# Kernel tuning notes

Hardware: AMD Instinct MI355X
Metric: run time of the kernel (lower is better)

## Reference

```python
import jax, jax.numpy as jnp
import numpy as np

H = 512          # hidden_size == input_size
K = 32768        # number of child cell inputs (lattice merge fan-in)


def setup_inputs() -> dict:
    key = jax.random.key(0)
    ks = jax.random.split(key, 8)
    s = 1.0 / np.sqrt(H)  # keep matmul outputs O(1)
    return {
        "input_": jax.random.normal(ks[0], (1, H), dtype=jnp.float32),
        "c_input": jax.random.normal(ks[1], (K, H), dtype=jnp.float32),
        "h_0": jax.random.normal(ks[2], (1, H), dtype=jnp.float32),
        "c_0": jax.random.normal(ks[3], (1, H), dtype=jnp.float32),
        "weight_ih": jax.random.normal(ks[4], (H, 3 * H), dtype=jnp.float32) * s,
        "weight_hh": jax.random.normal(ks[5], (H, 3 * H), dtype=jnp.float32) * s,
        "bias": jnp.zeros((3 * H,), dtype=jnp.float32),
        "alpha_weight_ih": jax.random.normal(ks[6], (H, H), dtype=jnp.float32) * s,
        "alpha_weight_hh": jax.random.normal(ks[7], (H, H), dtype=jnp.float32) * s,
    }


def reference(input_, c_input, h_0, c_0, weight_ih, weight_hh, bias,
              alpha_weight_ih, alpha_weight_hh):
    # Gate pre-activations: addmm(bias, h_0, W_hh) + input_ @ W_ih  -> [1, 3H]
    gates = h_0 @ weight_hh + bias + input_ @ weight_ih
    i, o, g = jnp.split(gates, 3, axis=1)        # each [1, H]
    i = jax.nn.sigmoid(i)
    o = jax.nn.sigmoid(o)
    g = jnp.tanh(g)

    # Variable-child softmax-weighted cell merge (non-empty c_input branch)
    alpha_wi = input_ @ alpha_weight_ih          # [1, H], broadcast over K
    alpha_wh = c_input @ alpha_weight_hh         # [K, H]
    alpha = jax.nn.sigmoid(alpha_wi + alpha_wh)  # [K, H]

    logits = jnp.concatenate([i, alpha], axis=0)  # [K+1, H]
    w = jnp.exp(logits)
    w = w / (w.sum(axis=0, keepdims=True) + 1e-12)

    merge = jnp.concatenate([g, c_input], axis=0)  # [K+1, H]
    c_1 = (merge * w).sum(axis=0, keepdims=True)   # [1, H]
    h_1 = o * jnp.tanh(c_1)                        # [1, H]
    return h_1, c_1
```

## Files before the change

### kernel.cpp

```cpp
#include <hip/hip_runtime.h>
#include <hip/hip_bf16.h>
#include <stdint.h>

#define Hdim 512
#define KC   32768

typedef __hip_bfloat16 bf16;
typedef __attribute__((ext_vector_type(8))) short short8;
typedef __attribute__((ext_vector_type(4))) float float4v;

__device__ __forceinline__ unsigned int pack_bf16_trunc(float e0, float e1) {
  union { float f; unsigned int u; } a, b;
  a.f = e0; b.f = e1;
  return __builtin_amdgcn_perm(b.u, a.u, 0x07060302u);
}

__global__ __launch_bounds__(256) void prep_wt_kernel(
    const float* __restrict__ input_, const float* __restrict__ h_0,
    const float* __restrict__ w_ih, const float* __restrict__ w_hh,
    const float* __restrict__ a_w_ih, const float* __restrict__ a_w_hh,
    float* __restrict__ gates, float* __restrict__ awi, bf16* __restrict__ wt) {
  __shared__ float sh[64 * 65];
  const int t = threadIdx.x;
  if (blockIdx.x < 128) {
    const int b  = blockIdx.x;
    const int jt = b & 31, dc = b >> 5;
    const int lane = t & 63, wv = t >> 6;
    float* h0s = sh;
    float* ins = sh + 128;
    float* red = sh + 256;
    if (t < 128) { h0s[t] = h_0[dc * 128 + t]; ins[t] = input_[dc * 128 + t]; }
    __syncthreads();
    float acc = 0.f;
    if (jt < 24) {
      const int j = jt * 64 + lane;
#pragma unroll 4
      for (int i = 0; i < 32; ++i) {
        const int dl = wv * 32 + i;
        const size_t d = dc * 128 + dl;
        acc += h0s[dl] * w_hh[d * 1536 + j] + ins[dl] * w_ih[d * 1536 + j];
      }
    } else {
      const int j = (jt - 24) * 64 + lane;
#pragma unroll 4
      for (int i = 0; i < 32; ++i) {
        const int dl = wv * 32 + i;
        const size_t d = dc * 128 + dl;
        acc += ins[dl] * a_w_ih[d * Hdim + j];
      }
    }
    red[wv * 64 + lane] = acc;
    __syncthreads();
    if (t < 64) {
      float s = red[t] + red[64 + t] + red[128 + t] + red[192 + t];
      if (jt < 24) atomicAdd(&gates[jt * 64 + t], s);
      else         atomicAdd(&awi[(jt - 24) * 64 + t], s);
    }
  } else {
    const int b = blockIdx.x - 128;
    const int d0 = (b & 7) * 64, h0 = (b >> 3) * 64;
    const int tx = t & 63, tw = t >> 6;
    float (*tile)[65] = (float (*)[65])sh;
#pragma unroll
    for (int r = 0; r < 16; ++r) {
      const int row = r * 4 + tw;
      tile[row][tx] = a_w_hh[(size_t)(d0 + row) * Hdim + h0 + tx];
    }
    __syncthreads();
#pragma unroll
    for (int r = 0; r < 16; ++r) {
      const int row = r * 4 + tw;
      wt[(size_t)(h0 + row) * Hdim + d0 + tx] = __float2bfloat16(tile[tx][row]);
    }
  }
}

__global__ __launch_bounds__(256) void gemm_reduce_kernel(
    const float* __restrict__ c_input, const bf16* __restrict__ WT,
    const float* __restrict__ awi,
    float* __restrict__ pw, float* __restrict__ pwc) {
  __shared__ __align__(16) bf16 As[128 * 64];
  __shared__ __align__(16) bf16 Bs[128 * 64];
  __shared__ float red_w[2][128];
  __shared__ float red_wc[2][128];

  const int tid  = threadIdx.x;
  const int lane = tid & 63;
  const int wave = tid >> 6;
  const int wm   = wave & 1;
  const int wn   = wave >> 1;
  const int lm   = lane & 15;
  const int lq   = lane >> 4;

  const int id     = blockIdx.x;
  const int kk_idx = ((id >> 5) << 3) | (id & 7);
  const int h_idx  = (id >> 3) & 3;
  const int kk0 = kk_idx * 128;
  const int h0  = h_idx * 128;

  float4v acc[4][4];
#pragma unroll
  for (int i = 0; i < 4; ++i)
#pragma unroll
    for (int j = 0; j < 4; ++j)
      acc[i][j] = (float4v){0.f, 0.f, 0.f, 0.f};

  char* AsB = (char*)As;
  char* BsB = (char*)Bs;

  for (int d0 = 0; d0 < Hdim; d0 += 64) {
#pragma unroll
    for (int j = 0; j < 8; ++j) {
      const int f = j * 256 + tid;
      const int row = f >> 4, sub = f & 15;
      float4v v = *(const float4v*)(c_input + (size_t)(kk0 + row) * Hdim + d0 + sub * 4);
      unsigned long long p = (unsigned long long)pack_bf16_trunc(v[0], v[1])
                           | ((unsigned long long)pack_bf16_trunc(v[2], v[3]) << 32);
      *(unsigned long long*)(AsB + row * 128 + (((sub >> 1) ^ (row & 7)) * 16) + (sub & 1) * 8) = p;
    }
#pragma unroll
    for (int r = 0; r < 4; ++r) {
      const int row = r * 32 + wave * 8 + (lane >> 3);
      const int g   = lane & 7;
      short8 wv8 = *(const short8*)(WT + (size_t)(h0 + row) * Hdim + d0 + g * 8);
      *(short8*)(BsB + row * 128 + ((g ^ (lane >> 3)) * 16)) = wv8;
    }
    __syncthreads();

#pragma unroll
    for (int ks = 0; ks < 2; ++ks) {
      short8 a[4], b[4];
#pragma unroll
      for (int mt = 0; mt < 4; ++mt) {
        const int row = wm * 64 + mt * 16 + lm;
        a[mt] = *(const short8*)(AsB + row * 128 + (((ks * 4 + lq) ^ (lm & 7)) * 16));
      }
#pragma unroll
      for (int nt = 0; nt < 4; ++nt) {
        const int row = wn * 64 + nt * 16 + lm;
        b[nt] = *(const short8*)(BsB + row * 128 + (((ks * 4 + lq) ^ (lm & 7)) * 16));
      }
#pragma unroll
      for (int mt = 0; mt < 4; ++mt)
#pragma unroll
        for (int nt = 0; nt < 4; ++nt)
          acc[mt][nt] = __builtin_amdgcn_mfma_f32_16x16x32_bf16(a[mt], b[nt], acc[mt][nt], 0, 0, 0);
    }
    __syncthreads();
  }

  float awi_l[4];
#pragma unroll
  for (int nt = 0; nt < 4; ++nt)
    awi_l[nt] = awi[h0 + wn * 64 + nt * 16 + lm];

  float sw[4] = {0.f, 0.f, 0.f, 0.f}, swc[4] = {0.f, 0.f, 0.f, 0.f};
#pragma unroll
  for (int nt = 0; nt < 4; ++nt) {
    const int h = h0 + wn * 64 + nt * 16 + lm;
#pragma unroll
    for (int mt = 0; mt < 4; ++mt) {
      const int kkb = kk0 + wm * 64 + mt * 16 + lq * 4;
#pragma unroll
      for (int r = 0; r < 4; ++r) {
        float v = acc[mt][nt][r] + awi_l[nt];
        float aval = 1.f / (1.f + __expf(-v));
        float e = __expf(aval);
        float c = c_input[(size_t)(kkb + r) * Hdim + h];
        sw[nt]  += e;
        swc[nt] += e * c;
      }
    }
  }
#pragma unroll
  for (int nt = 0; nt < 4; ++nt) {
    sw[nt]  += __shfl_xor(sw[nt], 16, 64);
    sw[nt]  += __shfl_xor(sw[nt], 32, 64);
    swc[nt] += __shfl_xor(swc[nt], 16, 64);
    swc[nt] += __shfl_xor(swc[nt], 32, 64);
  }
  if (lq == 0) {
#pragma unroll
    for (int nt = 0; nt < 4; ++nt) {
      red_w[wm][wn * 64 + nt * 16 + lm]  = sw[nt];
      red_wc[wm][wn * 64 + nt * 16 + lm] = swc[nt];
    }
  }
  __syncthreads();
  if (tid < 128) {
    pw[(size_t)kk_idx * Hdim + h0 + tid]  = red_w[0][tid] + red_w[1][tid];
    pwc[(size_t)kk_idx * Hdim + h0 + tid] = red_wc[0][tid] + red_wc[1][tid];
  }
}

__global__ __launch_bounds__(256) void finalize_kernel(
    const float* __restrict__ pw, const float* __restrict__ pwc,
    const float* __restrict__ gates, const float* __restrict__ bias,
    float* __restrict__ out) {
  __shared__ float rsw[4][64], rswc[4][64];
  const int t = threadIdx.x;
  const int hl = t & 63, q = t >> 6;
  const int hh = blockIdx.x * 64 + hl;
  float sw = 0.f, swc = 0.f;
#pragma unroll 4
  for (int kb = q * 64; kb < q * 64 + 64; ++kb) {
    sw  += pw[(size_t)kb * Hdim + hh];
    swc += pwc[(size_t)kb * Hdim + hh];
  }
  rsw[q][hl] = sw; rswc[q][hl] = swc;
  __syncthreads();
  if (t < 64) {
    const int h = blockIdx.x * 64 + t;
    sw  = rsw[0][t] + rsw[1][t] + rsw[2][t] + rsw[3][t];
    swc = rswc[0][t] + rswc[1][t] + rswc[2][t] + rswc[3][t];
    float ipre = gates[h] + bias[h];
    float opre = gates[Hdim + h] + bias[Hdim + h];
    float gpre = gates[2 * Hdim + h] + bias[2 * Hdim + h];
    float ei = expf(1.f / (1.f + expf(-ipre)));
    float g  = tanhf(gpre);
    float o  = 1.f / (1.f + expf(-opre));
    float denom = ei + sw + 1e-12f;
    float c1 = (ei * g + swc) / denom;
    float h1 = o * tanhf(c1);
    out[h]        = h1;
    out[Hdim + h] = c1;
  }
}

extern "C" void kernel_launch(void* const* d_in, const int* in_sizes, int n_in,
                              void* d_out, int out_size, void* d_ws, size_t ws_size,
                              hipStream_t stream) {
  const float* input_  = (const float*)d_in[0];
  const float* c_input = (const float*)d_in[1];
  const float* h_0     = (const float*)d_in[2];
  const float* w_ih    = (const float*)d_in[4];
  const float* w_hh    = (const float*)d_in[5];
  const float* bias    = (const float*)d_in[6];
  const float* a_w_ih  = (const float*)d_in[7];
  const float* a_w_hh  = (const float*)d_in[8];

  char* ws = (char*)d_ws;
  float* pw    = (float*)ws;
  float* pwc   = (float*)(ws + 512 * 1024);
  float* gates = (float*)(ws + 1024 * 1024);
  float* awi   = (float*)(ws + 1024 * 1024 + 6144);
  bf16*  WT    = (bf16*)(ws + 1024 * 1024 + 8192);

  hipMemsetAsync(ws + 1024 * 1024, 0, 8192, stream);
  hipLaunchKernelGGL(prep_wt_kernel, dim3(192), dim3(256), 0, stream,
                     input_, h_0, w_ih, w_hh, a_w_ih, a_w_hh, gates, awi, WT);
  hipLaunchKernelGGL(gemm_reduce_kernel, dim3(1024), dim3(256), 0, stream,
                     c_input, WT, awi, pw, pwc);
  hipLaunchKernelGGL(finalize_kernel, dim3(8), dim3(256), 0, stream,
                     pw, pwc, gates, bias, (float*)d_out);
}
```

Measured before the change: 152.6 us.

## Drop LDS staging in GEMM, load MFMA operands directly from global

The GEMM-reduce kernel drops its shared-memory tiling. Each wave now loads its 16-row A fragment straight from c_input, converts it to bf16, and reads B fragments for a 256-wide N slice directly from global memory. This removes the LDS round trips and the per-step barriers. In exchange, reuse of B across waves now relies on L1/L2 instead of LDS, and the number of partial-sum rows doubles. The prep kernel is also rewritten to compute the gate vectors with full 1024-thread blocks and no atomics, which removes the memset, and the finalize kernel reduces the partials with 16 waves.

```diff
diff --git a/kernel.cpp b/kernel.cpp
--- a/kernel.cpp
+++ b/kernel.cpp
@@ -15,61 +15,52 @@
   return __builtin_amdgcn_perm(b.u, a.u, 0x07060302u);
 }
 
-__global__ __launch_bounds__(256) void prep_wt_kernel(
+__global__ __launch_bounds__(1024) void prep_wt_kernel(
     const float* __restrict__ input_, const float* __restrict__ h_0,
     const float* __restrict__ w_ih, const float* __restrict__ w_hh,
     const float* __restrict__ a_w_ih, const float* __restrict__ a_w_hh,
     float* __restrict__ gates, float* __restrict__ awi, bf16* __restrict__ wt) {
-  __shared__ float sh[64 * 65];
   const int t = threadIdx.x;
-  if (blockIdx.x < 128) {
-    const int b  = blockIdx.x;
-    const int jt = b & 31, dc = b >> 5;
-    const int lane = t & 63, wv = t >> 6;
-    float* h0s = sh;
-    float* ins = sh + 128;
-    float* red = sh + 256;
-    if (t < 128) { h0s[t] = h_0[dc * 128 + t]; ins[t] = input_[dc * 128 + t]; }
+  if (blockIdx.x < 8) {
+    __shared__ float h0s[Hdim], ins[Hdim];
+    __shared__ float red[4][256];
+    const int js = t & 255, ds = t >> 8;
+    for (int i = t; i < Hdim; i += 1024) { h0s[i] = h_0[i]; ins[i] = input_[i]; }
     __syncthreads();
+    const int j = blockIdx.x * 256 + js;
     float acc = 0.f;
-    if (jt < 24) {
-      const int j = jt * 64 + lane;
-#pragma unroll 4
-      for (int i = 0; i < 32; ++i) {
-        const int dl = wv * 32 + i;
-        const size_t d = dc * 128 + dl;
-        acc += h0s[dl] * w_hh[d * 1536 + j] + ins[dl] * w_ih[d * 1536 + j];
-      }
+    if (j < 1536) {
+#pragma unroll 8
+      for (int d = ds * 128; d < ds * 128 + 128; ++d)
+        acc += h0s[d] * w_hh[(size_t)d * 1536 + j] + ins[d] * w_ih[(size_t)d * 1536 + j];
     } else {
-      const int j = (jt - 24) * 64 + lane;
-#pragma unroll 4
-      for (int i = 0; i < 32; ++i) {
-        const int dl = wv * 32 + i;
-        const size_t d = dc * 128 + dl;
-        acc += ins[dl] * a_w_ih[d * Hdim + j];
-      }
-    }
-    red[wv * 64 + lane] = acc;
+      const int jj = j - 1536;
+#pragma unroll 8
+      for (int d = ds * 128; d < ds * 128 + 128; ++d)
+        acc += ins[d] * a_w_ih[(size_t)d * Hdim + jj];
+    }
+    red[ds][js] = acc;
     __syncthreads();
-    if (t < 64) {
-      float s = red[t] + red[64 + t] + red[128 + t] + red[192 + t];
-      if (jt < 24) atomicAdd(&gates[jt * 64 + t], s);
-      else         atomicAdd(&awi[(jt - 24) * 64 + t], s);
+    if (t < 256) {
+      const int jo = blockIdx.x * 256 + t;
+      float s = red[0][t] + red[1][t] + red[2][t] + red[3][t];
+      if (jo < 1536) gates[jo] = s;
+      else           awi[jo - 1536] = s;
     }
   } else {
-    const int b = blockIdx.x - 128;
+    __shared__ float tile[64][65];
+    const int b = blockIdx.x - 8;
     const int d0 = (b & 7) * 64, h0 = (b >> 3) * 64;
     const int tx = t & 63, tw = t >> 6;
-    float (*tile)[65] = (float (*)[65])sh;
-#pragma unroll
-    for (int r = 0; r < 16; ++r) {
-      const int row = r * 4 + tw;
+#pragma unroll
+    for (int r = 0; r < 4; ++r) {
+      const int row = r * 16 + tw;
       tile[row][tx] = a_w_hh[(size_t)(d0 + row) * Hdim + h0 + tx];
     }
     __syncthreads();
 #pragma unroll
-    for (int r = 0; r < 16; ++r) {
-      const int row = r * 4 + tw;
+    for (int r = 0; r < 4; ++r) {
+      const int row = r * 16 + tw;
       wt[(size_t)(h0 + row) * Hdim + d0 + tx] = __float2bfloat16(tile[tx][row]);
     }
   }
@@ -79,131 +70,95 @@
     const float* __restrict__ c_input, const bf16* __restrict__ WT,
     const float* __restrict__ awi,
     float* __restrict__ pw, float* __restrict__ pwc) {
-  __shared__ __align__(16) bf16 As[128 * 64];
-  __shared__ __align__(16) bf16 Bs[128 * 64];
-  __shared__ float red_w[2][128];
-  __shared__ float red_wc[2][128];
+  __shared__ float red_w[4][256];
+  __shared__ float red_wc[4][256];
 
   const int tid  = threadIdx.x;
   const int lane = tid & 63;
-  const int wave = tid >> 6;
-  const int wm   = wave & 1;
-  const int wn   = wave >> 1;
+  const int wv   = tid >> 6;
   const int lm   = lane & 15;
   const int lq   = lane >> 4;
 
   const int id     = blockIdx.x;
-  const int kk_idx = ((id >> 5) << 3) | (id & 7);
-  const int h_idx  = (id >> 3) & 3;
-  const int kk0 = kk_idx * 128;
-  const int h0  = h_idx * 128;
-
-  float4v acc[4][4];
-#pragma unroll
-  for (int i = 0; i < 4; ++i)
-#pragma unroll
-    for (int j = 0; j < 4; ++j)
-      acc[i][j] = (float4v){0.f, 0.f, 0.f, 0.f};
-
-  char* AsB = (char*)As;
-  char* BsB = (char*)Bs;
-
-  for (int d0 = 0; d0 < Hdim; d0 += 64) {
-#pragma unroll
-    for (int j = 0; j < 8; ++j) {
-      const int f = j * 256 + tid;
-      const int row = f >> 4, sub = f & 15;
-      float4v v = *(const float4v*)(c_input + (size_t)(kk0 + row) * Hdim + d0 + sub * 4);
-      unsigned long long p = (unsigned long long)pack_bf16_trunc(v[0], v[1])
-                           | ((unsigned long long)pack_bf16_trunc(v[2], v[3]) << 32);
-      *(unsigned long long*)(AsB + row * 128 + (((sub >> 1) ^ (row & 7)) * 16) + (sub & 1) * 8) = p;
-    }
+  const int kk_idx = ((id >> 4) << 3) | (id & 7);
+  const int h_idx  = (id >> 3) & 1;
+  const int m0 = kk_idx * 64 + wv * 16;
+  const int n0 = h_idx * 256;
+
+  float4v acc[16];
+#pragma unroll
+  for (int i = 0; i < 16; ++i) acc[i] = (float4v){0.f, 0.f, 0.f, 0.f};
+
+  const float* arow = c_input + (size_t)(m0 + lm) * Hdim;
+
+#pragma unroll 2
+  for (int ks = 0; ks < 16; ++ks) {
+    const int kb = ks * 32 + lq * 8;
+    float4v a0 = *(const float4v*)(arow + kb);
+    float4v a1 = *(const float4v*)(arow + kb + 4);
+    union { unsigned int u[4]; short8 s; } af;
+    af.u[0] = pack_bf16_trunc(a0[0], a0[1]);
+    af.u[1] = pack_bf16_trunc(a0[2], a0[3]);
+    af.u[2] = pack_bf16_trunc(a1[0], a1[1]);
+    af.u[3] = pack_bf16_trunc(a1[2], a1[3]);
+    short8 bf0[8], bf1[8];
+#pragma unroll
+    for (int nt = 0; nt < 8; ++nt)
+      bf0[nt] = *(const short8*)(WT + (size_t)(n0 + nt * 16 + lm) * Hdim + kb);
+#pragma unroll
+    for (int nt = 0; nt < 8; ++nt)
+      acc[nt] = __builtin_amdgcn_mfma_f32_16x16x32_bf16(af.s, bf0[nt], acc[nt], 0, 0, 0);
+#pragma unroll
+    for (int nt = 0; nt < 8; ++nt)
+      bf1[nt] = *(const short8*)(WT + (size_t)(n0 + (nt + 8) * 16 + lm) * Hdim + kb);
+#pragma unroll
+    for (int nt = 0; nt < 8; ++nt)
+      acc[nt + 8] = __builtin_amdgcn_mfma_f32_16x16x32_bf16(af.s, bf1[nt], acc[nt + 8], 0, 0, 0);
+  }
+
+#pragma unroll
+  for (int nt = 0; nt < 16; ++nt) {
+    const int n = n0 + nt * 16 + lm;
+    const float aw = awi[n];
+    float sw = 0.f, swc = 0.f;
 #pragma unroll
     for (int r = 0; r < 4; ++r) {
-      const int row = r * 32 + wave * 8 + (lane >> 3);
-      const int g   = lane & 7;
-      short8 wv8 = *(const short8*)(WT + (size_t)(h0 + row) * Hdim + d0 + g * 8);
-      *(short8*)(BsB + row * 128 + ((g ^ (lane >> 3)) * 16)) = wv8;
-    }
-    __syncthreads();
-
-#pragma unroll
-    for (int ks = 0; ks < 2; ++ks) {
-      short8 a[4], b[4];
-#pragma unroll
-      for (int mt = 0; mt < 4; ++mt) {
-        const int row = wm * 64 + mt * 16 + lm;
-        a[mt] = *(const short8*)(AsB + row * 128 + (((ks * 4 + lq) ^ (lm & 7)) * 16));
-      }
-#pragma unroll
-      for (int nt = 0; nt < 4; ++nt) {
-        const int row = wn * 64 + nt * 16 + lm;
-        b[nt] = *(const short8*)(BsB + row * 128 + (((ks * 4 + lq) ^ (lm & 7)) * 16));
-      }
-#pragma unroll
-      for (int mt = 0; mt < 4; ++mt)
-#pragma unroll
-        for (int nt = 0; nt < 4; ++nt)
-          acc[mt][nt] = __builtin_amdgcn_mfma_f32_16x16x32_bf16(a[mt], b[nt], acc[mt][nt], 0, 0, 0);
-    }
-    __syncthreads();
-  }
-
-  float awi_l[4];
-#pragma unroll
-  for (int nt = 0; nt < 4; ++nt)
-    awi_l[nt] = awi[h0 + wn * 64 + nt * 16 + lm];
-
-  float sw[4] = {0.f, 0.f, 0.f, 0.f}, swc[4] = {0.f, 0.f, 0.f, 0.f};
-#pragma unroll
-  for (int nt = 0; nt < 4; ++nt) {
-    const int h = h0 + wn * 64 + nt * 16 + lm;
-#pragma unroll
-    for (int mt = 0; mt < 4; ++mt) {
-      const int kkb = kk0 + wm * 64 + mt * 16 + lq * 4;
-#pragma unroll
-      for (int r = 0; r < 4; ++r) {
-        float v = acc[mt][nt][r] + awi_l[nt];
-        float aval = 1.f / (1.f + __expf(-v));
-        float e = __expf(aval);
-        float c = c_input[(size_t)(kkb + r) * Hdim + h];
-        sw[nt]  += e;
-        swc[nt] += e * c;
-      }
-    }
-  }
-#pragma unroll
-  for (int nt = 0; nt < 4; ++nt) {
-    sw[nt]  += __shfl_xor(sw[nt], 16, 64);
-    sw[nt]  += __shfl_xor(sw[nt], 32, 64);
-    swc[nt] += __shfl_xor(swc[nt], 16, 64);
-    swc[nt] += __shfl_xor(swc[nt], 32, 64);
-  }
-  if (lq == 0) {
-#pragma unroll
-    for (int nt = 0; nt < 4; ++nt) {
-      red_w[wm][wn * 64 + nt * 16 + lm]  = sw[nt];
-      red_wc[wm][wn * 64 + nt * 16 + lm] = swc[nt];
+      float v = acc[nt][r] + aw;
+      float alpha = 1.f / (1.f + __expf(-v));
+      float e = __expf(alpha);
+      float c = c_input[(size_t)(m0 + lq * 4 + r) * Hdim + n];
+      sw  += e;
+      swc += e * c;
+    }
+    sw  += __shfl_xor(sw, 16, 64);
+    sw  += __shfl_xor(sw, 32, 64);
+    swc += __shfl_xor(swc, 16, 64);
+    swc += __shfl_xor(swc, 32, 64);
+    if (lq == 0) {
+      red_w[wv][nt * 16 + lm]  = sw;
+      red_wc[wv][nt * 16 + lm] = swc;
     }
   }
   __syncthreads();
-  if (tid < 128) {
-    pw[(size_t)kk_idx * Hdim + h0 + tid]  = red_w[0][tid] + red_w[1][tid];
-    pwc[(size_t)kk_idx * Hdim + h0 + tid] = red_wc[0][tid] + red_wc[1][tid];
-  }
-}
-
-__global__ __launch_bounds__(256) void finalize_kernel(
+  {
+    float s  = red_w[0][tid] + red_w[1][tid] + red_w[2][tid] + red_w[3][tid];
+    float sc = red_wc[0][tid] + red_wc[1][tid] + red_wc[2][tid] + red_wc[3][tid];
+    pw[(size_t)kk_idx * Hdim + n0 + tid]  = s;
+    pwc[(size_t)kk_idx * Hdim + n0 + tid] = sc;
+  }
+}
+
+__global__ __launch_bounds__(1024) void finalize_kernel(
     const float* __restrict__ pw, const float* __restrict__ pwc,
     const float* __restrict__ gates, const float* __restrict__ bias,
     float* __restrict__ out) {
-  __shared__ float rsw[4][64], rswc[4][64];
+  __shared__ float rsw[16][64], rswc[16][64];
   const int t = threadIdx.x;
   const int hl = t & 63, q = t >> 6;
   const int hh = blockIdx.x * 64 + hl;
   float sw = 0.f, swc = 0.f;
-#pragma unroll 4
-  for (int kb = q * 64; kb < q * 64 + 64; ++kb) {
+#pragma unroll 8
+  for (int kb = q * 32; kb < q * 32 + 32; ++kb) {
     sw  += pw[(size_t)kb * Hdim + hh];
     swc += pwc[(size_t)kb * Hdim + hh];
   }
@@ -211,8 +166,9 @@
   __syncthreads();
   if (t < 64) {
     const int h = blockIdx.x * 64 + t;
-    sw  = rsw[0][t] + rsw[1][t] + rsw[2][t] + rsw[3][t];
-    swc = rswc[0][t] + rswc[1][t] + rswc[2][t] + rswc[3][t];
+    sw = 0.f; swc = 0.f;
+#pragma unroll
+    for (int qq = 0; qq < 16; ++qq) { sw += rsw[qq][t]; swc += rswc[qq][t]; }
     float ipre = gates[h] + bias[h];
     float opre = gates[Hdim + h] + bias[Hdim + h];
     float gpre = gates[2 * Hdim + h] + bias[2 * Hdim + h];
@@ -241,16 +197,15 @@
 
   char* ws = (char*)d_ws;
   float* pw    = (float*)ws;
-  float* pwc   = (float*)(ws + 512 * 1024);
-  float* gates = (float*)(ws + 1024 * 1024);
-  float* awi   = (float*)(ws + 1024 * 1024 + 6144);
-  bf16*  WT    = (bf16*)(ws + 1024 * 1024 + 8192);
-
-  hipMemsetAsync(ws + 1024 * 1024, 0, 8192, stream);
-  hipLaunchKernelGGL(prep_wt_kernel, dim3(192), dim3(256), 0, stream,
+  float* pwc   = (float*)(ws + 1024 * 1024);
+  float* gates = (float*)(ws + 2 * 1024 * 1024);
+  float* awi   = (float*)(ws + 2 * 1024 * 1024 + 6144);
+  bf16*  WT    = (bf16*)(ws + 2 * 1024 * 1024 + 8192);
+
+  hipLaunchKernelGGL(prep_wt_kernel, dim3(72), dim3(1024), 0, stream,
                      input_, h_0, w_ih, w_hh, a_w_ih, a_w_hh, gates, awi, WT);
   hipLaunchKernelGGL(gemm_reduce_kernel, dim3(1024), dim3(256), 0, stream,
                      c_input, WT, awi, pw, pwc);
-  hipLaunchKernelGGL(finalize_kernel, dim3(8), dim3(256), 0, stream,
+  hipLaunchKernelGGL(finalize_kernel, dim3(8), dim3(1024), 0, stream,
                      pw, pwc, gates, bias, (float*)d_out);
 }
```

Result: slower. 256.8 us (+68.3%).

## Register-prefetch next GEMM tile, drop memset/atomics, widen prep and finalize blocks

Applied to the files above, without the earlier changes.

The main GEMM loop now loads the next 64-column slice of c_input and WT into registers while MFMAs run on the current shared-memory tile. This hides global-load latency behind compute, with one barrier per iteration instead of two. The prep kernel uses 1024-thread blocks that cover the whole reduction dimension, so gates and awi are written directly and the memset and atomics go away. Finalize uses 1024 threads per block to spread the partial-sum reduction. The cost is higher register pressure from the prefetch buffers in the GEMM kernel.

```diff
diff --git a/kernel.cpp b/kernel.cpp
--- a/kernel.cpp
+++ b/kernel.cpp
@@ -8,6 +8,7 @@
 typedef __hip_bfloat16 bf16;
 typedef __attribute__((ext_vector_type(8))) short short8;
 typedef __attribute__((ext_vector_type(4))) float float4v;
+typedef __attribute__((ext_vector_type(4))) unsigned int uint4v;
 
 __device__ __forceinline__ unsigned int pack_bf16_trunc(float e0, float e1) {
   union { float f; unsigned int u; } a, b;
@@ -15,61 +16,52 @@
   return __builtin_amdgcn_perm(b.u, a.u, 0x07060302u);
 }
 
-__global__ __launch_bounds__(256) void prep_wt_kernel(
+__global__ __launch_bounds__(1024) void prep_wt_kernel(
     const float* __restrict__ input_, const float* __restrict__ h_0,
     const float* __restrict__ w_ih, const float* __restrict__ w_hh,
     const float* __restrict__ a_w_ih, const float* __restrict__ a_w_hh,
     float* __restrict__ gates, float* __restrict__ awi, bf16* __restrict__ wt) {
-  __shared__ float sh[64 * 65];
   const int t = threadIdx.x;
-  if (blockIdx.x < 128) {
-    const int b  = blockIdx.x;
-    const int jt = b & 31, dc = b >> 5;
-    const int lane = t & 63, wv = t >> 6;
-    float* h0s = sh;
-    float* ins = sh + 128;
-    float* red = sh + 256;
-    if (t < 128) { h0s[t] = h_0[dc * 128 + t]; ins[t] = input_[dc * 128 + t]; }
-    __syncthreads();
+  if (blockIdx.x < 8) {
+    __shared__ float h0s[Hdim], ins[Hdim];
+    __shared__ float red[4][256];
+    const int js = t & 255, ds = t >> 8;
+    for (int i = t; i < Hdim; i += 1024) { h0s[i] = h_0[i]; ins[i] = input_[i]; }
+    __syncthreads();
+    const int j = blockIdx.x * 256 + js;
     float acc = 0.f;
-    if (jt < 24) {
-      const int j = jt * 64 + lane;
-#pragma unroll 4
-      for (int i = 0; i < 32; ++i) {
-        const int dl = wv * 32 + i;
-        const size_t d = dc * 128 + dl;
-        acc += h0s[dl] * w_hh[d * 1536 + j] + ins[dl] * w_ih[d * 1536 + j];
-      }
+    if (j < 1536) {
+#pragma unroll 8
+      for (int d = ds * 128; d < ds * 128 + 128; ++d)
+        acc += h0s[d] * w_hh[(size_t)d * 1536 + j] + ins[d] * w_ih[(size_t)d * 1536 + j];
     } else {
-      const int j = (jt - 24) * 64 + lane;
-#pragma unroll 4
-      for (int i = 0; i < 32; ++i) {
-        const int dl = wv * 32 + i;
-        const size_t d = dc * 128 + dl;
-        acc += ins[dl] * a_w_ih[d * Hdim + j];
-      }
-    }
-    red[wv * 64 + lane] = acc;
-    __syncthreads();
-    if (t < 64) {
-      float s = red[t] + red[64 + t] + red[128 + t] + red[192 + t];
-      if (jt < 24) atomicAdd(&gates[jt * 64 + t], s);
-      else         atomicAdd(&awi[(jt - 24) * 64 + t], s);
+      const int jj = j - 1536;
+#pragma unroll 8
+      for (int d = ds * 128; d < ds * 128 + 128; ++d)
+        acc += ins[d] * a_w_ih[(size_t)d * Hdim + jj];
+    }
+    red[ds][js] = acc;
+    __syncthreads();
+    if (t < 256) {
+      const int jo = blockIdx.x * 256 + t;
+      float s = red[0][t] + red[1][t] + red[2][t] + red[3][t];
+      if (jo < 1536) gates[jo] = s;
+      else           awi[jo - 1536] = s;
     }
   } else {
-    const int b = blockIdx.x - 128;
+    __shared__ float tile[64][65];
+    const int b = blockIdx.x - 8;
     const int d0 = (b & 7) * 64, h0 = (b >> 3) * 64;
     const int tx = t & 63, tw = t >> 6;
-    float (*tile)[65] = (float (*)[65])sh;
-#pragma unroll
-    for (int r = 0; r < 16; ++r) {
-      const int row = r * 4 + tw;
+#pragma unroll
+    for (int r = 0; r < 4; ++r) {
+      const int row = r * 16 + tw;
       tile[row][tx] = a_w_hh[(size_t)(d0 + row) * Hdim + h0 + tx];
     }
     __syncthreads();
 #pragma unroll
-    for (int r = 0; r < 16; ++r) {
-      const int row = r * 4 + tw;
+    for (int r = 0; r < 4; ++r) {
+      const int row = r * 16 + tw;
       wt[(size_t)(h0 + row) * Hdim + d0 + tx] = __float2bfloat16(tile[tx][row]);
     }
   }
@@ -86,9 +78,9 @@
 
   const int tid  = threadIdx.x;
   const int lane = tid & 63;
-  const int wave = tid >> 6;
-  const int wm   = wave & 1;
-  const int wn   = wave >> 1;
+  const int wv   = tid >> 6;
+  const int wm   = wv & 1;
+  const int wn   = wv >> 1;
   const int lm   = lane & 15;
   const int lq   = lane >> 4;
 
@@ -98,6 +90,13 @@
   const int kk0 = kk_idx * 128;
   const int h0  = h_idx * 128;
 
+  const int ar_base = tid >> 3;
+  const int acol    = (tid & 7) * 8;
+  const int aga     = tid & 7;
+  const int br_base = wv * 8 + (lane >> 3);
+  const int bg      = (lane & 7) ^ (lane >> 3);
+  const int bcol    = (lane & 7) * 8;
+
   float4v acc[4][4];
 #pragma unroll
   for (int i = 0; i < 4; ++i)
@@ -108,25 +107,49 @@
   char* AsB = (char*)As;
   char* BsB = (char*)Bs;
 
-  for (int d0 = 0; d0 < Hdim; d0 += 64) {
-#pragma unroll
-    for (int j = 0; j < 8; ++j) {
-      const int f = j * 256 + tid;
-      const int row = f >> 4, sub = f & 15;
-      float4v v = *(const float4v*)(c_input + (size_t)(kk0 + row) * Hdim + d0 + sub * 4);
-      unsigned long long p = (unsigned long long)pack_bf16_trunc(v[0], v[1])
-                           | ((unsigned long long)pack_bf16_trunc(v[2], v[3]) << 32);
-      *(unsigned long long*)(AsB + row * 128 + (((sub >> 1) ^ (row & 7)) * 16) + (sub & 1) * 8) = p;
+  float4v pa0[4], pa1[4];
+  short8  pb[4];
+#pragma unroll
+  for (int j = 0; j < 4; ++j) {
+    const float* p = c_input + (size_t)(kk0 + j * 32 + ar_base) * Hdim + acol;
+    pa0[j] = *(const float4v*)p;
+    pa1[j] = *(const float4v*)(p + 4);
+  }
+#pragma unroll
+  for (int r = 0; r < 4; ++r)
+    pb[r] = *(const short8*)(WT + (size_t)(h0 + r * 32 + br_base) * Hdim + bcol);
+
+#pragma unroll 1
+  for (int it = 0; it < 8; ++it) {
+    __syncthreads();
+#pragma unroll
+    for (int j = 0; j < 4; ++j) {
+      const int row = j * 32 + ar_base;
+      uint4v u;
+      u[0] = pack_bf16_trunc(pa0[j][0], pa0[j][1]);
+      u[1] = pack_bf16_trunc(pa0[j][2], pa0[j][3]);
+      u[2] = pack_bf16_trunc(pa1[j][0], pa1[j][1]);
+      u[3] = pack_bf16_trunc(pa1[j][2], pa1[j][3]);
+      *(uint4v*)(AsB + row * 128 + ((aga ^ (row & 7)) * 16)) = u;
     }
 #pragma unroll
     for (int r = 0; r < 4; ++r) {
-      const int row = r * 32 + wave * 8 + (lane >> 3);
-      const int g   = lane & 7;
-      short8 wv8 = *(const short8*)(WT + (size_t)(h0 + row) * Hdim + d0 + g * 8);
-      *(short8*)(BsB + row * 128 + ((g ^ (lane >> 3)) * 16)) = wv8;
-    }
-    __syncthreads();
-
+      const int row = r * 32 + br_base;
+      *(short8*)(BsB + row * 128 + bg * 16) = pb[r];
+    }
+    __syncthreads();
+    if (it < 7) {
+      const int d0 = (it + 1) * 64;
+#pragma unroll
+      for (int j = 0; j < 4; ++j) {
+        const float* p = c_input + (size_t)(kk0 + j * 32 + ar_base) * Hdim + d0 + acol;
+        pa0[j] = *(const float4v*)p;
+        pa1[j] = *(const float4v*)(p + 4);
+      }
+#pragma unroll
+      for (int r = 0; r < 4; ++r)
+        pb[r] = *(const short8*)(WT + (size_t)(h0 + r * 32 + br_base) * Hdim + d0 + bcol);
+    }
 #pragma unroll
     for (int ks = 0; ks < 2; ++ks) {
       short8 a[4], b[4];
@@ -146,7 +169,6 @@
         for (int nt = 0; nt < 4; ++nt)
           acc[mt][nt] = __builtin_amdgcn_mfma_f32_16x16x32_bf16(a[mt], b[nt], acc[mt][nt], 0, 0, 0);
     }
-    __syncthreads();
   }
 
   float awi_l[4];
@@ -164,8 +186,8 @@
 #pragma unroll
       for (int r = 0; r < 4; ++r) {
         float v = acc[mt][nt][r] + awi_l[nt];
-        float aval = 1.f / (1.f + __expf(-v));
-        float e = __expf(aval);
+        float alpha = 1.f / (1.f + __expf(-v));
+        float e = __expf(alpha);
         float c = c_input[(size_t)(kkb + r) * Hdim + h];
         sw[nt]  += e;
         swc[nt] += e * c;
@@ -193,17 +215,17 @@
   }
 }
 
-__global__ __launch_bounds__(256) void finalize_kernel(
+__global__ __launch_bounds__(1024) void finalize_kernel(
     const float* __restrict__ pw, const float* __restrict__ pwc,
     const float* __restrict__ gates, const float* __restrict__ bias,
     float* __restrict__ out) {
-  __shared__ float rsw[4][64], rswc[4][64];
+  __shared__ float rsw[16][64], rswc[16][64];
   const int t = threadIdx.x;
   const int hl = t & 63, q = t >> 6;
   const int hh = blockIdx.x * 64 + hl;
   float sw = 0.f, swc = 0.f;
-#pragma unroll 4
-  for (int kb = q * 64; kb < q * 64 + 64; ++kb) {
+#pragma unroll 8
+  for (int kb = q * 16; kb < q * 16 + 16; ++kb) {
     sw  += pw[(size_t)kb * Hdim + hh];
     swc += pwc[(size_t)kb * Hdim + hh];
   }
@@ -211,8 +233,9 @@
   __syncthreads();
   if (t < 64) {
     const int h = blockIdx.x * 64 + t;
-    sw  = rsw[0][t] + rsw[1][t] + rsw[2][t] + rsw[3][t];
-    swc = rswc[0][t] + rswc[1][t] + rswc[2][t] + rswc[3][t];
+    sw = 0.f; swc = 0.f;
+#pragma unroll
+    for (int qq = 0; qq < 16; ++qq) { sw += rsw[qq][t]; swc += rswc[qq][t]; }
     float ipre = gates[h] + bias[h];
     float opre = gates[Hdim + h] + bias[Hdim + h];
     float gpre = gates[2 * Hdim + h] + bias[2 * Hdim + h];
@@ -246,11 +269,10 @@
   float* awi   = (float*)(ws + 1024 * 1024 + 6144);
   bf16*  WT    = (bf16*)(ws + 1024 * 1024 + 8192);
 
-  hipMemsetAsync(ws + 1024 * 1024, 0, 8192, stream);
-  hipLaunchKernelGGL(prep_wt_kernel, dim3(192), dim3(256), 0, stream,
+  hipLaunchKernelGGL(prep_wt_kernel, dim3(72), dim3(1024), 0, stream,
                      input_, h_0, w_ih, w_hh, a_w_ih, a_w_hh, gates, awi, WT);
   hipLaunchKernelGGL(gemm_reduce_kernel, dim3(1024), dim3(256), 0, stream,
                      c_input, WT, awi, pw, pwc);
-  hipLaunchKernelGGL(finalize_kernel, dim3(8), dim3(256), 0, stream,
+  hipLaunchKernelGGL(finalize_kernel, dim3(8), dim3(1024), 0, stream,
                      pw, pwc, gates, bias, (float*)d_out);
 }
```

New measurement: 154.1 us. Within noise of the previous version (+1.0%).

## Use single-wave 64x64 GEMM tiles, drop the memset and atomics, widen finalize

Applied to the files above, without the earlier changes.

The GEMM+reduce kernel changes from 256-thread blocks with 128x128 tiles and block barriers to one-wave blocks computing 64x64 tiles. Each block stages 32-wide K chunks through small swizzled LDS buffers without __syncthreads, and the grid grows to 4096 blocks. This aims to remove barrier stalls and raise occupancy, but c_input is now read for eight column groups instead of four. The prep kernel now writes per-chunk partial sums, which makes the memset and atomics unnecessary, and the finalize kernel uses 1024 threads to reduce the doubled number of partial rows.

```diff
diff --git a/kernel.cpp b/kernel.cpp
--- a/kernel.cpp
+++ b/kernel.cpp
@@ -8,6 +8,7 @@
 typedef __hip_bfloat16 bf16;
 typedef __attribute__((ext_vector_type(8))) short short8;
 typedef __attribute__((ext_vector_type(4))) float float4v;
+typedef __attribute__((ext_vector_type(4))) unsigned int uint4v;
 
 __device__ __forceinline__ unsigned int pack_bf16_trunc(float e0, float e1) {
   union { float f; unsigned int u; } a, b;
@@ -19,16 +20,15 @@
     const float* __restrict__ input_, const float* __restrict__ h_0,
     const float* __restrict__ w_ih, const float* __restrict__ w_hh,
     const float* __restrict__ a_w_ih, const float* __restrict__ a_w_hh,
-    float* __restrict__ gates, float* __restrict__ awi, bf16* __restrict__ wt) {
-  __shared__ float sh[64 * 65];
+    float* __restrict__ gates_part, float* __restrict__ awi_part,
+    bf16* __restrict__ wt) {
   const int t = threadIdx.x;
   if (blockIdx.x < 128) {
-    const int b  = blockIdx.x;
+    __shared__ float h0s[128], ins[128];
+    __shared__ float red[4][64];
+    const int b = blockIdx.x;
     const int jt = b & 31, dc = b >> 5;
     const int lane = t & 63, wv = t >> 6;
-    float* h0s = sh;
-    float* ins = sh + 128;
-    float* red = sh + 256;
     if (t < 128) { h0s[t] = h_0[dc * 128 + t]; ins[t] = input_[dc * 128 + t]; }
     __syncthreads();
     float acc = 0.f;
@@ -49,18 +49,18 @@
         acc += ins[dl] * a_w_ih[d * Hdim + j];
       }
     }
-    red[wv * 64 + lane] = acc;
+    red[wv][lane] = acc;
     __syncthreads();
     if (t < 64) {
-      float s = red[t] + red[64 + t] + red[128 + t] + red[192 + t];
-      if (jt < 24) atomicAdd(&gates[jt * 64 + t], s);
-      else         atomicAdd(&awi[(jt - 24) * 64 + t], s);
+      float s = red[0][t] + red[1][t] + red[2][t] + red[3][t];
+      if (jt < 24) gates_part[dc * 1536 + jt * 64 + t] = s;
+      else         awi_part[dc * Hdim + (jt - 24) * 64 + t] = s;
     }
   } else {
+    __shared__ float tile[64][65];
     const int b = blockIdx.x - 128;
     const int d0 = (b & 7) * 64, h0 = (b >> 3) * 64;
     const int tx = t & 63, tw = t >> 6;
-    float (*tile)[65] = (float (*)[65])sh;
 #pragma unroll
     for (int r = 0; r < 16; ++r) {
       const int row = r * 4 + tw;
@@ -75,28 +75,22 @@
   }
 }
 
-__global__ __launch_bounds__(256) void gemm_reduce_kernel(
+__global__ __launch_bounds__(64, 4) void gemm_reduce_kernel(
     const float* __restrict__ c_input, const bf16* __restrict__ WT,
-    const float* __restrict__ awi,
+    const float* __restrict__ awi_part,
     float* __restrict__ pw, float* __restrict__ pwc) {
-  __shared__ __align__(16) bf16 As[128 * 64];
-  __shared__ __align__(16) bf16 Bs[128 * 64];
-  __shared__ float red_w[2][128];
-  __shared__ float red_wc[2][128];
-
-  const int tid  = threadIdx.x;
-  const int lane = tid & 63;
-  const int wave = tid >> 6;
-  const int wm   = wave & 1;
-  const int wn   = wave >> 1;
-  const int lm   = lane & 15;
-  const int lq   = lane >> 4;
-
-  const int id     = blockIdx.x;
-  const int kk_idx = ((id >> 5) << 3) | (id & 7);
-  const int h_idx  = (id >> 3) & 3;
-  const int kk0 = kk_idx * 128;
-  const int h0  = h_idx * 128;
+  __shared__ __align__(16) char AsB[64 * 64];
+  __shared__ __align__(16) char BsB[64 * 64];
+
+  const int lane = threadIdx.x;
+  const int lm = lane & 15, lq = lane >> 4;
+  const int id = blockIdx.x;
+  const int mg = ((id >> 6) << 3) | (id & 7);
+  const int ng = (id >> 3) & 7;
+  const int m0 = mg * 64, n0 = ng * 64;
+
+  const int sr = lane >> 2;
+  const int sg = lane & 3;
 
   float4v acc[4][4];
 #pragma unroll
@@ -105,105 +99,82 @@
     for (int j = 0; j < 4; ++j)
       acc[i][j] = (float4v){0.f, 0.f, 0.f, 0.f};
 
-  char* AsB = (char*)As;
-  char* BsB = (char*)Bs;
-
-  for (int d0 = 0; d0 < Hdim; d0 += 64) {
-#pragma unroll
-    for (int j = 0; j < 8; ++j) {
-      const int f = j * 256 + tid;
-      const int row = f >> 4, sub = f & 15;
-      float4v v = *(const float4v*)(c_input + (size_t)(kk0 + row) * Hdim + d0 + sub * 4);
-      unsigned long long p = (unsigned long long)pack_bf16_trunc(v[0], v[1])
-                           | ((unsigned long long)pack_bf16_trunc(v[2], v[3]) << 32);
-      *(unsigned long long*)(AsB + row * 128 + (((sub >> 1) ^ (row & 7)) * 16) + (sub & 1) * 8) = p;
-    }
+#pragma unroll 2
+  for (int kc = 0; kc < 16; ++kc) {
+    const int k0 = kc * 32;
 #pragma unroll
     for (int r = 0; r < 4; ++r) {
-      const int row = r * 32 + wave * 8 + (lane >> 3);
-      const int g   = lane & 7;
-      short8 wv8 = *(const short8*)(WT + (size_t)(h0 + row) * Hdim + d0 + g * 8);
-      *(short8*)(BsB + row * 128 + ((g ^ (lane >> 3)) * 16)) = wv8;
-    }
-    __syncthreads();
-
-#pragma unroll
-    for (int ks = 0; ks < 2; ++ks) {
-      short8 a[4], b[4];
-#pragma unroll
-      for (int mt = 0; mt < 4; ++mt) {
-        const int row = wm * 64 + mt * 16 + lm;
-        a[mt] = *(const short8*)(AsB + row * 128 + (((ks * 4 + lq) ^ (lm & 7)) * 16));
+      const int row = r * 16 + sr;
+      const float* p = c_input + (size_t)(m0 + row) * Hdim + k0 + sg * 8;
+      float4v v0 = *(const float4v*)p;
+      float4v v1 = *(const float4v*)(p + 4);
+      uint4v u;
+      u[0] = pack_bf16_trunc(v0[0], v0[1]);
+      u[1] = pack_bf16_trunc(v0[2], v0[3]);
+      u[2] = pack_bf16_trunc(v1[0], v1[1]);
+      u[3] = pack_bf16_trunc(v1[2], v1[3]);
+      *(uint4v*)(AsB + row * 64 + ((sg ^ (row & 3)) << 4)) = u;
+    }
+#pragma unroll
+    for (int r = 0; r < 4; ++r) {
+      const int row = r * 16 + sr;
+      *(short8*)(BsB + row * 64 + ((sg ^ (row & 3)) << 4)) =
+          *(const short8*)(WT + (size_t)(n0 + row) * Hdim + k0 + sg * 8);
+    }
+    short8 a[4], b[4];
+#pragma unroll
+    for (int mt = 0; mt < 4; ++mt)
+      a[mt] = *(const short8*)(AsB + (mt * 16 + lm) * 64 + ((lq ^ (lm & 3)) << 4));
+#pragma unroll
+    for (int nt = 0; nt < 4; ++nt)
+      b[nt] = *(const short8*)(BsB + (nt * 16 + lm) * 64 + ((lq ^ (lm & 3)) << 4));
+#pragma unroll
+    for (int mt = 0; mt < 4; ++mt)
+#pragma unroll
+      for (int nt = 0; nt < 4; ++nt)
+        acc[mt][nt] = __builtin_amdgcn_mfma_f32_16x16x32_bf16(a[mt], b[nt], acc[mt][nt], 0, 0, 0);
+  }
+
+#pragma unroll
+  for (int nt = 0; nt < 4; ++nt) {
+    const int n = n0 + nt * 16 + lm;
+    float aw = awi_part[n] + awi_part[Hdim + n] + awi_part[2 * Hdim + n] + awi_part[3 * Hdim + n];
+    float sw = 0.f, swc = 0.f;
+#pragma unroll
+    for (int mt = 0; mt < 4; ++mt) {
+      const int mrow = m0 + mt * 16 + lq * 4;
+#pragma unroll
+      for (int r = 0; r < 4; ++r) {
+        float v = acc[mt][nt][r] + aw;
+        float alpha = 1.f / (1.f + __expf(-v));
+        float e = __expf(alpha);
+        float c = c_input[(size_t)(mrow + r) * Hdim + n];
+        sw  += e;
+        swc += e * c;
       }
-#pragma unroll
-      for (int nt = 0; nt < 4; ++nt) {
-        const int row = wn * 64 + nt * 16 + lm;
-        b[nt] = *(const short8*)(BsB + row * 128 + (((ks * 4 + lq) ^ (lm & 7)) * 16));
-      }
-#pragma unroll
-      for (int mt = 0; mt < 4; ++mt)
-#pragma unroll
-        for (int nt = 0; nt < 4; ++nt)
-          acc[mt][nt] = __builtin_amdgcn_mfma_f32_16x16x32_bf16(a[mt], b[nt], acc[mt][nt], 0, 0, 0);
-    }
-    __syncthreads();
-  }
-
-  float awi_l[4];
-#pragma unroll
-  for (int nt = 0; nt < 4; ++nt)
-    awi_l[nt] = awi[h0 + wn * 64 + nt * 16 + lm];
-
-  float sw[4] = {0.f, 0.f, 0.f, 0.f}, swc[4] = {0.f, 0.f, 0.f, 0.f};
-#pragma unroll
-  for (int nt = 0; nt < 4; ++nt) {
-    const int h = h0 + wn * 64 + nt * 16 + lm;
-#pragma unroll
-    for (int mt = 0; mt < 4; ++mt) {
-      const int kkb = kk0 + wm * 64 + mt * 16 + lq * 4;
-#pragma unroll
-      for (int r = 0; r < 4; ++r) {
-        float v = acc[mt][nt][r] + awi_l[nt];
-        float aval = 1.f / (1.f + __expf(-v));
-        float e = __expf(aval);
-        float c = c_input[(size_t)(kkb + r) * Hdim + h];
-        sw[nt]  += e;
-        swc[nt] += e * c;
-      }
-    }
-  }
-#pragma unroll
-  for (int nt = 0; nt < 4; ++nt) {
-    sw[nt]  += __shfl_xor(sw[nt], 16, 64);
-    sw[nt]  += __shfl_xor(sw[nt], 32, 64);
-    swc[nt] += __shfl_xor(swc[nt], 16, 64);
-    swc[nt] += __shfl_xor(swc[nt], 32, 64);
-  }
-  if (lq == 0) {
-#pragma unroll
-    for (int nt = 0; nt < 4; ++nt) {
-      red_w[wm][wn * 64 + nt * 16 + lm]  = sw[nt];
-      red_wc[wm][wn * 64 + nt * 16 + lm] = swc[nt];
-    }
-  }
-  __syncthreads();
-  if (tid < 128) {
-    pw[(size_t)kk_idx * Hdim + h0 + tid]  = red_w[0][tid] + red_w[1][tid];
-    pwc[(size_t)kk_idx * Hdim + h0 + tid] = red_wc[0][tid] + red_wc[1][tid];
-  }
-}
-
-__global__ __launch_bounds__(256) void finalize_kernel(
+    }
+    sw  += __shfl_xor(sw, 16, 64);
+    sw  += __shfl_xor(sw, 32, 64);
+    swc += __shfl_xor(swc, 16, 64);
+    swc += __shfl_xor(swc, 32, 64);
+    if (lq == 0) {
+      pw[(size_t)mg * Hdim + n]  = sw;
+      pwc[(size_t)mg * Hdim + n] = swc;
+    }
+  }
+}
+
+__global__ __launch_bounds__(1024) void finalize_kernel(
     const float* __restrict__ pw, const float* __restrict__ pwc,
-    const float* __restrict__ gates, const float* __restrict__ bias,
+    const float* __restrict__ gates_part, const float* __restrict__ bias,
     float* __restrict__ out) {
-  __shared__ float rsw[4][64], rswc[4][64];
+  __shared__ float rsw[16][64], rswc[16][64];
   const int t = threadIdx.x;
   const int hl = t & 63, q = t >> 6;
   const int hh = blockIdx.x * 64 + hl;
   float sw = 0.f, swc = 0.f;
-#pragma unroll 4
-  for (int kb = q * 64; kb < q * 64 + 64; ++kb) {
+#pragma unroll 8
+  for (int kb = q * 32; kb < q * 32 + 32; ++kb) {
     sw  += pw[(size_t)kb * Hdim + hh];
     swc += pwc[(size_t)kb * Hdim + hh];
   }
@@ -211,11 +182,17 @@
   __syncthreads();
   if (t < 64) {
     const int h = blockIdx.x * 64 + t;
-    sw  = rsw[0][t] + rsw[1][t] + rsw[2][t] + rsw[3][t];
-    swc = rswc[0][t] + rswc[1][t] + rswc[2][t] + rswc[3][t];
-    float ipre = gates[h] + bias[h];
-    float opre = gates[Hdim + h] + bias[Hdim + h];
-    float gpre = gates[2 * Hdim + h] + bias[2 * Hdim + h];
+    sw = 0.f; swc = 0.f;
+#pragma unroll
+    for (int qq = 0; qq < 16; ++qq) { sw += rsw[qq][t]; swc += rswc[qq][t]; }
+    float ipre = gates_part[h] + gates_part[1536 + h] + gates_part[2 * 1536 + h]
+               + gates_part[3 * 1536 + h] + bias[h];
+    float opre = gates_part[Hdim + h] + gates_part[1536 + Hdim + h]
+               + gates_part[2 * 1536 + Hdim + h] + gates_part[3 * 1536 + Hdim + h]
+               + bias[Hdim + h];
+    float gpre = gates_part[2 * Hdim + h] + gates_part[1536 + 2 * Hdim + h]
+               + gates_part[2 * 1536 + 2 * Hdim + h] + gates_part[3 * 1536 + 2 * Hdim + h]
+               + bias[2 * Hdim + h];
     float ei = expf(1.f / (1.f + expf(-ipre)));
     float g  = tanhf(gpre);
     float o  = 1.f / (1.f + expf(-opre));
@@ -240,17 +217,16 @@
   const float* a_w_hh  = (const float*)d_in[8];
 
   char* ws = (char*)d_ws;
-  float* pw    = (float*)ws;
-  float* pwc   = (float*)(ws + 512 * 1024);
-  float* gates = (float*)(ws + 1024 * 1024);
-  float* awi   = (float*)(ws + 1024 * 1024 + 6144);
-  bf16*  WT    = (bf16*)(ws + 1024 * 1024 + 8192);
-
-  hipMemsetAsync(ws + 1024 * 1024, 0, 8192, stream);
+  float* pw         = (float*)ws;
+  float* pwc        = (float*)(ws + 1024 * 1024);
+  float* gates_part = (float*)(ws + 2 * 1024 * 1024);
+  float* awi_part   = (float*)(ws + 2 * 1024 * 1024 + 24576);
+  bf16*  WT         = (bf16*)(ws + 2 * 1024 * 1024 + 32768);
+
   hipLaunchKernelGGL(prep_wt_kernel, dim3(192), dim3(256), 0, stream,
-                     input_, h_0, w_ih, w_hh, a_w_ih, a_w_hh, gates, awi, WT);
-  hipLaunchKernelGGL(gemm_reduce_kernel, dim3(1024), dim3(256), 0, stream,
-                     c_input, WT, awi, pw, pwc);
-  hipLaunchKernelGGL(finalize_kernel, dim3(8), dim3(256), 0, stream,
-                     pw, pwc, gates, bias, (float*)d_out);
-}
+                     input_, h_0, w_ih, w_hh, a_w_ih, a_w_hh, gates_part, awi_part, WT);
+  hipLaunchKernelGGL(gemm_reduce_kernel, dim3(4096), dim3(64), 0, stream,
+                     c_input, WT, awi_part, pw, pwc);
+  hipLaunchKernelGGL(finalize_kernel, dim3(8), dim3(1024), 0, stream,
+                     pw, pwc, gates_part, bias, (float*)d_out);
+}
```

New measurement: 186.3 us. 22.1% more time.
